# Optimization experiments

Hardware: AMD Instinct MI355X
Metric: run time of the kernel (lower is better)

## Reference

```python
import jax, jax.numpy as jnp
import numpy as np

B, S, F = 4096, 512, 128
D = 2 * F  # inner_depth = num_features * 2

def _gelu(x):
    # torch nn.GELU() default is exact (erf) form
    return jax.nn.gelu(x, approximate=False)

def setup_inputs() -> dict:
    key = jax.random.key(0)
    ks = jax.random.split(key, 10)
    w = lambda k, shp: (jax.random.normal(k, shp) * 0.05).astype(jnp.float32)
    z = lambda n: jnp.zeros((n,), jnp.float32)
    return dict(
        noise=jax.random.normal(ks[0], (B, F), dtype=jnp.float32),   # torch.randn(batch,1,F) squeezed
        eps=jax.random.normal(ks[1], (S, B, F), dtype=jnp.float32),  # rsample noise per step
        mlp_w1=w(ks[2], (F, F)), mlp_b1=z(F),
        mlp_w2=w(ks[3], (F, F)), mlp_b2=z(F),
        mlp_w3=w(ks[4], (F, F)), mlp_b3=z(F),
        hid_w=w(ks[5], (D, F)), hid_b=z(D),
        w_ih=w(ks[6], (4 * D, F)), b_ih=z(4 * D),   # PyTorch LSTM gate order: i, f, g, o
        w_hh=w(ks[7], (4 * D, D)), b_hh=z(4 * D),
        out_w=w(ks[8], (F, D)), out_b=z(F),
        z_w=w(ks[9], (2 * F, F)), z_b=z(2 * F),     # ConditionalGaussian linear -> (mu, logsigma)
        batch=B, seq_len=S,
    )

def _forward(noise, eps, mlp_w1, mlp_b1, mlp_w2, mlp_b2, mlp_w3, mlp_b3,
             hid_w, hid_b, w_ih, b_ih, w_hh, b_hh, out_w, out_b, z_w, z_b):
    # noise_mlp: Linear -> GELU -> Linear -> GELU -> Linear
    x = _gelu(noise @ mlp_w1.T + mlp_b1)
    x = _gelu(x @ mlp_w2.T + mlp_b2)
    inputs = x @ mlp_w3.T + mlp_b3          # [B, F]
    hidden = inputs @ hid_w.T + hid_b       # [B, D]
    cell = jnp.tanh(hidden)
    b = b_ih + b_hh

    def step(carry, eps_t):
        inp, h, c = carry
        gates = inp @ w_ih.T + h @ w_hh.T + b               # [B, 4D]
        i, f, g, o = jnp.split(gates, 4, axis=-1)
        c = jax.nn.sigmoid(f) * c + jax.nn.sigmoid(i) * jnp.tanh(g)
        h = jax.nn.sigmoid(o) * jnp.tanh(c)
        out = h @ out_w.T + out_b                           # [B, F]
        # ConditionalGaussian: GELU -> Linear -> chunk -> rsample (temperature=1)
        mu, logsigma = jnp.split(_gelu(out) @ z_w.T + z_b, 2, axis=-1)
        sample = mu + jnp.exp(logsigma) * eps_t             # [B, F]
        return (sample, h, c), sample

    _, ys = jax.lax.scan(step, (inputs, hidden, cell), eps)  # ys: [S, B, F]
    return jnp.transpose(ys, (1, 0, 2))  # stack(dim=1) -> [B, S, F]

def reference(noise, eps, mlp_w1, mlp_b1, mlp_w2, mlp_b2, mlp_w3, mlp_b3,
              hid_w, hid_b, w_ih, b_ih, w_hh, b_hh, out_w, out_b, z_w, z_b,
              batch, seq_len):
    return _forward(noise, eps, mlp_w1, mlp_b1, mlp_w2, mlp_b2, mlp_w3, mlp_b3,
                    hid_w, hid_b, w_ih, b_ih, w_hh, b_hh, out_w, out_b, z_w, z_b)
```

## Files before the change

kernel.cpp:

```cpp
#include <hip/hip_runtime.h>
#include <hip/hip_bf16.h>
#include <math.h>

#define BATCH 4096
#define SEQ   512
#define FDIM  128
#define DDIM  256
#define KG    384
#define NG    1024

typedef __bf16 bf16x8 __attribute__((ext_vector_type(8)));
typedef float  f32x4  __attribute__((ext_vector_type(4)));

__device__ __forceinline__ f32x4 mfma16(bf16x8 a, bf16x8 b, f32x4 c) {
    return __builtin_amdgcn_mfma_f32_16x16x32_bf16(a, b, c, 0, 0, 0);
}

__device__ __forceinline__ float rcp_(float x) { return __builtin_amdgcn_rcpf(x); }
__device__ __forceinline__ float sigmoid_(float x) { return rcp_(1.0f + __expf(-x)); }
__device__ __forceinline__ float tanh_(float x) {
    float e = __expf(-2.0f * fabsf(x));
    float t = 1.0f - 2.0f * e * rcp_(1.0f + e);
    return copysignf(t, x);
}
__device__ __forceinline__ float gelu_erf(float v) {
    return 0.5f * v * (1.0f + erff(v * 0.70710678118654752f));
}

__global__ void prep_weights(const float* __restrict__ w_ih, const float* __restrict__ w_hh,
                             const float* __restrict__ b_ih, const float* __restrict__ b_hh,
                             const float* __restrict__ out_w, const float* __restrict__ z_w,
                             __bf16* __restrict__ Wg, __bf16* __restrict__ Wout,
                             __bf16* __restrict__ Wz, float* __restrict__ bg)
{
    int i = blockIdx.x * blockDim.x + threadIdx.x;
    if (i < NG * KG) {
        int n = i / KG, k = i - n * KG;
        float v = (k < FDIM) ? w_ih[n * FDIM + k] : w_hh[n * DDIM + (k - FDIM)];
        Wg[i] = (__bf16)v;
    }
    if (i < FDIM * DDIM) Wout[i] = (__bf16)out_w[i];
    if (i < DDIM * FDIM) Wz[i]   = (__bf16)z_w[i];
    if (i < NG)          bg[i]   = b_ih[i] + b_hh[i];
}

template<int K, int N, int ACT>
__global__ void rowmlp(const float* __restrict__ x, const float* __restrict__ W,
                       const float* __restrict__ bias, float* __restrict__ y)
{
    __shared__ float xr[K];
    int m = blockIdx.x;
    for (int k = threadIdx.x; k < K; k += blockDim.x) xr[k] = x[(size_t)m * K + k];
    __syncthreads();
    for (int n = threadIdx.x; n < N; n += blockDim.x) {
        const float* wr = W + (size_t)n * K;
        float s = bias[n];
        #pragma unroll 8
        for (int k = 0; k < K; ++k) s += xr[k] * wr[k];
        if (ACT) s = gelu_erf(s);
        y[(size_t)m * N + n] = s;
    }
}

__global__ __launch_bounds__(512, 2)
void rnn_main(const float* __restrict__ eps,
              const __bf16* __restrict__ Wg, const float* __restrict__ bg,
              const __bf16* __restrict__ Wout, const float* __restrict__ ob,
              const __bf16* __restrict__ Wz, const float* __restrict__ zb,
              const float* __restrict__ x0, const float* __restrict__ h0,
              float* __restrict__ out)
{
    extern __shared__ __align__(16) char smem[];
    __bf16* xbuf  = (__bf16*)smem;
    __bf16* hbufA = xbuf  + 2048;
    __bf16* hbufB = hbufA + 4096;
    __bf16* gbuf  = hbufB + 4096;
    char*   wlds  = (char*)(gbuf + 2048);

    const int tid  = threadIdx.x;
    const int wv   = tid >> 6;
    const int lane = tid & 63;
    const int lo   = lane & 15;
    const int hi   = lane >> 4;
    const int row0 = blockIdx.x * 16;
    const int abase = (hi * 16 + lo) * 16;

    for (int e = tid; e < 16 * 128; e += 512) {
        int r = e >> 7, k = e & 127;
        xbuf[(((k >> 3) << 4) + r) * 8 + (k & 7)] = (__bf16)x0[(size_t)(row0 + r) * 128 + k];
    }
    for (int e = tid; e < 16 * 256; e += 512) {
        int r = e >> 8, k = e & 255;
        hbufA[(((k >> 3) << 4) + r) * 8 + (k & 7)] = (__bf16)h0[(size_t)(row0 + r) * 256 + k];
    }
    float c[2][4];
    #pragma unroll
    for (int p = 0; p < 2; ++p)
        #pragma unroll
        for (int j = 0; j < 4; ++j)
            c[p][j] = tanh_(h0[(size_t)(row0 + hi * 4 + j) * 256 + (2 * wv + p) * 16 + lo]);

    const __bf16* wgbase[8];
    float biasq[8];
    #pragma unroll
    for (int q = 0; q < 8; ++q) {
        int tile = (q >> 1) * 16 + 2 * wv + (q & 1);
        wgbase[q] = Wg + (size_t)(tile * 16 + lo) * KG + hi * 8;
        biasq[q]  = bg[tile * 16 + lo];
    }
    const float bo  = ob[wv * 16 + lo];
    const float bmu = zb[wv * 16 + lo];
    const float bls = zb[128 + wv * 16 + lo];

    bf16x8 wout[8];
    #pragma unroll
    for (int kt = 0; kt < 8; ++kt)
        wout[kt] = *(const bf16x8*)(Wout + (size_t)(wv * 16 + lo) * 256 + kt * 32 + hi * 8);
    bf16x8 wz0[4], wz1[4];
    #pragma unroll
    for (int kt = 0; kt < 4; ++kt) {
        wz0[kt] = *(const bf16x8*)(Wz + (size_t)(wv * 16 + lo) * 128 + kt * 32 + hi * 8);
        wz1[kt] = *(const bf16x8*)(Wz + (size_t)((8 + wv) * 16 + lo) * 128 + kt * 32 + hi * 8);
    }
    bf16x8 wgr[2][8];
    #pragma unroll
    for (int q = 0; q < 8; ++q) {
        wgr[0][q] = *(const bf16x8*)(wgbase[q] + 10 * 32);
        wgr[1][q] = *(const bf16x8*)(wgbase[q] + 11 * 32);
    }
    char* wbase = wlds + wv * 8192 + lane * 16;
    #pragma unroll
    for (int kt2 = 0; kt2 < 2; ++kt2)
        #pragma unroll
        for (int q = 0; q < 8; ++q) {
            bf16x8 w = *(const bf16x8*)(wgbase[q] + (8 + kt2) * 32);
            *(bf16x8*)(wbase + kt2 * 65536 + q * 1024) = w;
        }

    __syncthreads();

    __bf16* hb_cur = hbufA;
    __bf16* hb_nxt = hbufB;

    for (int t = 0; t < SEQ; ++t) {
        float ev[4];
        #pragma unroll
        for (int j = 0; j < 4; ++j)
            ev[j] = eps[((size_t)t * BATCH + row0 + hi * 4 + j) * 128 + wv * 16 + lo];

        f32x4 acc[8];
        #pragma unroll
        for (int q = 0; q < 8; ++q) acc[q] = (f32x4){biasq[q], biasq[q], biasq[q], biasq[q]};

        #pragma unroll 2
        for (int kt = 0; kt < 4; ++kt) {
            bf16x8 a = *(const bf16x8*)((char*)xbuf + kt * 1024 + abase);
            #pragma unroll
            for (int q = 0; q < 8; ++q) {
                bf16x8 b = *(const bf16x8*)(wgbase[q] + kt * 32);
                acc[q] = mfma16(a, b, acc[q]);
            }
        }
        #pragma unroll 2
        for (int kt = 0; kt < 4; ++kt) {
            bf16x8 a = *(const bf16x8*)((char*)hb_cur + kt * 1024 + abase);
            #pragma unroll
            for (int q = 0; q < 8; ++q) {
                bf16x8 b = *(const bf16x8*)(wgbase[q] + (4 + kt) * 32);
                acc[q] = mfma16(a, b, acc[q]);
            }
        }
        #pragma unroll
        for (int kt2 = 0; kt2 < 2; ++kt2) {
            bf16x8 a = *(const bf16x8*)((char*)hb_cur + (4 + kt2) * 1024 + abase);
            #pragma unroll
            for (int q = 0; q < 8; ++q) {
                bf16x8 b = *(const bf16x8*)(wbase + kt2 * 65536 + q * 1024);
                acc[q] = mfma16(a, b, acc[q]);
            }
        }
        #pragma unroll
        for (int kt2 = 0; kt2 < 2; ++kt2) {
            bf16x8 a = *(const bf16x8*)((char*)hb_cur + (6 + kt2) * 1024 + abase);
            #pragma unroll
            for (int q = 0; q < 8; ++q)
                acc[q] = mfma16(a, wgr[kt2][q], acc[q]);
        }

        #pragma unroll
        for (int p = 0; p < 2; ++p)
            #pragma unroll
            for (int j = 0; j < 4; ++j) {
                float iv = sigmoid_(acc[0 + p][j]);
                float fv = sigmoid_(acc[2 + p][j]);
                float gv = tanh_(acc[4 + p][j]);
                float ov = sigmoid_(acc[6 + p][j]);
                float cn = fv * c[p][j] + iv * gv;
                c[p][j] = cn;
                float hv = ov * tanh_(cn);
                int d = (2 * wv + p) * 16 + lo, r = hi * 4 + j;
                hb_nxt[(((d >> 3) << 4) + r) * 8 + (d & 7)] = (__bf16)hv;
            }
        __syncthreads();

        f32x4 ao0 = (f32x4){bo, bo, bo, bo};
        f32x4 ao1 = (f32x4){0.f, 0.f, 0.f, 0.f};
        #pragma unroll
        for (int kt = 0; kt < 4; ++kt) {
            bf16x8 a0 = *(const bf16x8*)((char*)hb_nxt + (2 * kt) * 1024 + abase);
            bf16x8 a1 = *(const bf16x8*)((char*)hb_nxt + (2 * kt + 1) * 1024 + abase);
            ao0 = mfma16(a0, wout[2 * kt], ao0);
            ao1 = mfma16(a1, wout[2 * kt + 1], ao1);
        }
        #pragma unroll
        for (int j = 0; j < 4; ++j) {
            int d = wv * 16 + lo, r = hi * 4 + j;
            gbuf[(((d >> 3) << 4) + r) * 8 + (d & 7)] = (__bf16)gelu_erf(ao0[j] + ao1[j]);
        }
        __syncthreads();

        f32x4 amu = (f32x4){bmu, bmu, bmu, bmu};
        f32x4 als = (f32x4){bls, bls, bls, bls};
        #pragma unroll
        for (int kt = 0; kt < 4; ++kt) {
            bf16x8 a = *(const bf16x8*)((char*)gbuf + kt * 1024 + abase);
            amu = mfma16(a, wz0[kt], amu);
            als = mfma16(a, wz1[kt], als);
        }
        #pragma unroll
        for (int j = 0; j < 4; ++j) {
            float smp = amu[j] + __expf(als[j]) * ev[j];
            int d = wv * 16 + lo, r = hi * 4 + j;
            xbuf[(((d >> 3) << 4) + r) * 8 + (d & 7)] = (__bf16)smp;
            out[(size_t)(row0 + r) * (SEQ * 128) + (size_t)t * 128 + d] = smp;
        }
        __syncthreads();

        __bf16* tmp = hb_cur; hb_cur = hb_nxt; hb_nxt = tmp;
    }
}

extern "C" void kernel_launch(void* const* d_in, const int* in_sizes, int n_in,
                              void* d_out, int out_size, void* d_ws, size_t ws_size,
                              hipStream_t stream)
{
    const float* noise = (const float*)d_in[0];
    const float* eps   = (const float*)d_in[1];
    const float* w1 = (const float*)d_in[2];  const float* b1 = (const float*)d_in[3];
    const float* w2 = (const float*)d_in[4];  const float* b2 = (const float*)d_in[5];
    const float* w3 = (const float*)d_in[6];  const float* b3 = (const float*)d_in[7];
    const float* hw = (const float*)d_in[8];  const float* hb = (const float*)d_in[9];
    const float* wih = (const float*)d_in[10]; const float* bih = (const float*)d_in[11];
    const float* whh = (const float*)d_in[12]; const float* bhh = (const float*)d_in[13];
    const float* ow = (const float*)d_in[14]; const float* ob = (const float*)d_in[15];
    const float* zw = (const float*)d_in[16]; const float* zb = (const float*)d_in[17];
    float* out = (float*)d_out;

    char* ws = (char*)d_ws;
    __bf16* Wg   = (__bf16*)(ws);
    __bf16* Wout = (__bf16*)(ws + 786432);
    __bf16* Wz   = (__bf16*)(ws + 851968);
    float*  bg   = (float*) (ws + 917504);
    float*  t0   = (float*) (ws + 921600);
    float*  t1   = (float*) (ws + 921600 + 2097152);
    float*  hid  = (float*) (ws + 921600 + 2 * 2097152);

    prep_weights<<<1536, 256, 0, stream>>>(wih, whh, bih, bhh, ow, zw, Wg, Wout, Wz, bg);

    rowmlp<128, 128, 1><<<4096, 128, 0, stream>>>(noise, w1, b1, t0);
    rowmlp<128, 128, 1><<<4096, 128, 0, stream>>>(t0, w2, b2, t1);
    rowmlp<128, 128, 0><<<4096, 128, 0, stream>>>(t1, w3, b3, t0);
    rowmlp<128, 256, 0><<<4096, 256, 0, stream>>>(t0, hw, hb, hid);

    rnn_main<<<256, 512, 155648, stream>>>(eps, Wg, bg, Wout, ob, Wz, zb, t0, hid, out);
}
```

Measured before the change: 9.900 ms.

## Stream gate weight k-tiles via async global-to-LDS double buffering with rotated order

Replaces direct global loads of gate weight tiles inside the MFMA loop with global_load_lds staging into two LDS buffers. Each k-tile's weights are prefetched two iterations ahead, and each block starts at a different k offset to spread L2 traffic. Barriers become lightweight lgkmcnt waits plus s_barrier, and erff is replaced by a polynomial erf approximation. This adds manual vmcnt bookkeeping, a looser GELU approximation (about 1e-7 error), and extra LDS traffic every step.

```diff
diff --git a/kernel.cpp b/kernel.cpp
--- a/kernel.cpp
+++ b/kernel.cpp
@@ -23,8 +23,16 @@
     float t = 1.0f - 2.0f * e * rcp_(1.0f + e);
     return copysignf(t, x);
 }
+__device__ __forceinline__ float erf_(float x) {
+    float ax = fabsf(x);
+    float t  = rcp_(fmaf(0.3275911f, ax, 1.0f));
+    float y  = t * fmaf(t, fmaf(t, fmaf(t, fmaf(t, 1.061405429f, -1.453152027f),
+                                        1.421413741f), -0.284496736f), 0.254829592f);
+    float r  = 1.0f - y * __expf(-ax * ax);
+    return copysignf(r, x);
+}
 __device__ __forceinline__ float gelu_erf(float v) {
-    return 0.5f * v * (1.0f + erff(v * 0.70710678118654752f));
+    return 0.5f * v * (1.0f + erf_(v * 0.70710678118654752f));
 }
 
 __global__ void prep_weights(const float* __restrict__ w_ih, const float* __restrict__ w_hh,
@@ -62,6 +70,13 @@
     }
 }
 
+__device__ __forceinline__ void bar_lds() {
+    asm volatile("s_waitcnt lgkmcnt(0)" ::: "memory");
+    __builtin_amdgcn_sched_barrier(0);
+    __builtin_amdgcn_s_barrier();
+    __builtin_amdgcn_sched_barrier(0);
+}
+
 __global__ __launch_bounds__(512, 2)
 void rnn_main(const float* __restrict__ eps,
               const __bf16* __restrict__ Wg, const float* __restrict__ bg,
@@ -72,10 +87,10 @@
 {
     extern __shared__ __align__(16) char smem[];
     __bf16* xbuf  = (__bf16*)smem;
-    __bf16* hbufA = xbuf  + 2048;
-    __bf16* hbufB = hbufA + 4096;
-    __bf16* gbuf  = hbufB + 4096;
-    char*   wlds  = (char*)(gbuf + 2048);
+    __bf16* hbufA = (__bf16*)(smem + 4096);
+    __bf16* hbufB = (__bf16*)(smem + 12288);
+    __bf16* gbuf  = (__bf16*)(smem + 20480);
+    char*   wlds  = smem + 24576;
 
     const int tid  = threadIdx.x;
     const int wv   = tid >> 6;
@@ -128,64 +143,91 @@
         wgr[0][q] = *(const bf16x8*)(wgbase[q] + 10 * 32);
         wgr[1][q] = *(const bf16x8*)(wgbase[q] + 11 * 32);
     }
-    char* wbase = wlds + wv * 8192 + lane * 16;
-    #pragma unroll
-    for (int kt2 = 0; kt2 < 2; ++kt2)
-        #pragma unroll
-        for (int q = 0; q < 8; ++q) {
-            bf16x8 w = *(const bf16x8*)(wgbase[q] + (8 + kt2) * 32);
-            *(bf16x8*)(wbase + kt2 * 65536 + q * 1024) = w;
-        }
-
+
+    const int rot = blockIdx.x % 10;
+    #define KTV(I) ((rot + (I)) < 10 ? (rot + (I)) : (rot + (I) - 10))
+    const int kt_0 = KTV(0), kt_1 = KTV(1), kt_2 = KTV(2), kt_3 = KTV(3), kt_4 = KTV(4);
+    const int kt_5 = KTV(5), kt_6 = KTV(6), kt_7 = KTV(7), kt_8 = KTV(8), kt_9 = KTV(9);
+    const int kts0 = kt_2, kts1 = kt_3, kts2 = kt_4, kts3 = kt_5, kts4 = kt_6;
+    const int kts5 = kt_7, kts6 = kt_8, kts7 = kt_9, kts8 = kt_0, kts9 = kt_1;
+
+    #define STAGE8(KTS, PAR) do {                                                         \
+        char* sd_ = wlds + (PAR) * 65536 + wv * 8192;                                     \
+        _Pragma("unroll")                                                                 \
+        for (int q = 0; q < 8; ++q) {                                                     \
+            __builtin_amdgcn_global_load_lds(                                             \
+                (const __attribute__((address_space(1))) unsigned int*)(const void*)(wgbase[q] + (KTS) * 32), \
+                (__attribute__((address_space(3))) unsigned int*)(void*)(sd_ + q * 1024), \
+                16, 0, 0);                                                                \
+        }                                                                                 \
+    } while (0)
+
+    #define GITER(I, VM) do {                                                             \
+        asm volatile("s_waitcnt vmcnt(" #VM ")" ::: "memory");                            \
+        __builtin_amdgcn_sched_barrier(0);                                                \
+        const char* rb_ = wlds + ((I) & 1) * 65536 + wv * 8192 + lane * 16;               \
+        bf16x8 a_  = *(const bf16x8*)(aptr##I + abase);                                   \
+        bf16x8 b0_ = *(const bf16x8*)(rb_ + 0 * 1024);                                    \
+        bf16x8 b1_ = *(const bf16x8*)(rb_ + 1 * 1024);                                    \
+        bf16x8 b2_ = *(const bf16x8*)(rb_ + 2 * 1024);                                    \
+        bf16x8 b3_ = *(const bf16x8*)(rb_ + 3 * 1024);                                    \
+        bf16x8 b4_ = *(const bf16x8*)(rb_ + 4 * 1024);                                    \
+        bf16x8 b5_ = *(const bf16x8*)(rb_ + 5 * 1024);                                    \
+        bf16x8 b6_ = *(const bf16x8*)(rb_ + 6 * 1024);                                    \
+        bf16x8 b7_ = *(const bf16x8*)(rb_ + 7 * 1024);                                    \
+        asm volatile("s_waitcnt lgkmcnt(0)" ::: "memory");                                \
+        __builtin_amdgcn_sched_barrier(0);                                                \
+        STAGE8(kts##I, (I) & 1);                                                          \
+        acc[0] = mfma16(a_, b0_, acc[0]);                                                 \
+        acc[1] = mfma16(a_, b1_, acc[1]);                                                 \
+        acc[2] = mfma16(a_, b2_, acc[2]);                                                 \
+        acc[3] = mfma16(a_, b3_, acc[3]);                                                 \
+        acc[4] = mfma16(a_, b4_, acc[4]);                                                 \
+        acc[5] = mfma16(a_, b5_, acc[5]);                                                 \
+        acc[6] = mfma16(a_, b6_, acc[6]);                                                 \
+        acc[7] = mfma16(a_, b7_, acc[7]);                                                 \
+    } while (0)
+
+    STAGE8(kt_0, 0);
+    STAGE8(kt_1, 1);
+    asm volatile("s_waitcnt vmcnt(0)" ::: "memory");
     __syncthreads();
 
-    __bf16* hb_cur = hbufA;
-    __bf16* hb_nxt = hbufB;
+    __bf16* hc = hbufA;
+    __bf16* hn = hbufB;
 
     for (int t = 0; t < SEQ; ++t) {
+        #define APTR(K) ((K) < 4 ? (const char*)xbuf + (K) * 1024 : (const char*)hc + ((K) - 4) * 1024)
+        const char* aptr0 = APTR(kt_0); const char* aptr1 = APTR(kt_1);
+        const char* aptr2 = APTR(kt_2); const char* aptr3 = APTR(kt_3);
+        const char* aptr4 = APTR(kt_4); const char* aptr5 = APTR(kt_5);
+        const char* aptr6 = APTR(kt_6); const char* aptr7 = APTR(kt_7);
+        const char* aptr8 = APTR(kt_8); const char* aptr9 = APTR(kt_9);
+        #undef APTR
+
         float ev[4];
         #pragma unroll
         for (int j = 0; j < 4; ++j)
             ev[j] = eps[((size_t)t * BATCH + row0 + hi * 4 + j) * 128 + wv * 16 + lo];
+        __builtin_amdgcn_sched_barrier(0);
 
         f32x4 acc[8];
         #pragma unroll
         for (int q = 0; q < 8; ++q) acc[q] = (f32x4){biasq[q], biasq[q], biasq[q], biasq[q]};
 
-        #pragma unroll 2
-        for (int kt = 0; kt < 4; ++kt) {
-            bf16x8 a = *(const bf16x8*)((char*)xbuf + kt * 1024 + abase);
+        {
+            bf16x8 a10 = *(const bf16x8*)((const char*)hc + 6 * 1024 + abase);
+            bf16x8 a11 = *(const bf16x8*)((const char*)hc + 7 * 1024 + abase);
             #pragma unroll
-            for (int q = 0; q < 8; ++q) {
-                bf16x8 b = *(const bf16x8*)(wgbase[q] + kt * 32);
-                acc[q] = mfma16(a, b, acc[q]);
-            }
-        }
-        #pragma unroll 2
-        for (int kt = 0; kt < 4; ++kt) {
-            bf16x8 a = *(const bf16x8*)((char*)hb_cur + kt * 1024 + abase);
+            for (int q = 0; q < 8; ++q) acc[q] = mfma16(a10, wgr[0][q], acc[q]);
             #pragma unroll
-            for (int q = 0; q < 8; ++q) {
-                bf16x8 b = *(const bf16x8*)(wgbase[q] + (4 + kt) * 32);
-                acc[q] = mfma16(a, b, acc[q]);
-            }
-        }
-        #pragma unroll
-        for (int kt2 = 0; kt2 < 2; ++kt2) {
-            bf16x8 a = *(const bf16x8*)((char*)hb_cur + (4 + kt2) * 1024 + abase);
-            #pragma unroll
-            for (int q = 0; q < 8; ++q) {
-                bf16x8 b = *(const bf16x8*)(wbase + kt2 * 65536 + q * 1024);
-                acc[q] = mfma16(a, b, acc[q]);
-            }
-        }
-        #pragma unroll
-        for (int kt2 = 0; kt2 < 2; ++kt2) {
-            bf16x8 a = *(const bf16x8*)((char*)hb_cur + (6 + kt2) * 1024 + abase);
-            #pragma unroll
-            for (int q = 0; q < 8; ++q)
-                acc[q] = mfma16(a, wgr[kt2][q], acc[q]);
-        }
+            for (int q = 0; q < 8; ++q) acc[q] = mfma16(a11, wgr[1][q], acc[q]);
+        }
+
+        GITER(0, 16); GITER(1, 16);
+        asm volatile("" : "+v"(ev[0]), "+v"(ev[1]), "+v"(ev[2]), "+v"(ev[3]));
+        GITER(2, 8); GITER(3, 8); GITER(4, 8); GITER(5, 8);
+        GITER(6, 8); GITER(7, 8); GITER(8, 8); GITER(9, 8);
 
         #pragma unroll
         for (int p = 0; p < 2; ++p)
@@ -199,16 +241,16 @@
                 c[p][j] = cn;
                 float hv = ov * tanh_(cn);
                 int d = (2 * wv + p) * 16 + lo, r = hi * 4 + j;
-                hb_nxt[(((d >> 3) << 4) + r) * 8 + (d & 7)] = (__bf16)hv;
+                hn[(((d >> 3) << 4) + r) * 8 + (d & 7)] = (__bf16)hv;
             }
-        __syncthreads();
+        bar_lds();
 
         f32x4 ao0 = (f32x4){bo, bo, bo, bo};
         f32x4 ao1 = (f32x4){0.f, 0.f, 0.f, 0.f};
         #pragma unroll
         for (int kt = 0; kt < 4; ++kt) {
-            bf16x8 a0 = *(const bf16x8*)((char*)hb_nxt + (2 * kt) * 1024 + abase);
-            bf16x8 a1 = *(const bf16x8*)((char*)hb_nxt + (2 * kt + 1) * 1024 + abase);
+            bf16x8 a0 = *(const bf16x8*)((const char*)hn + (2 * kt) * 1024 + abase);
+            bf16x8 a1 = *(const bf16x8*)((const char*)hn + (2 * kt + 1) * 1024 + abase);
             ao0 = mfma16(a0, wout[2 * kt], ao0);
             ao1 = mfma16(a1, wout[2 * kt + 1], ao1);
         }
@@ -217,13 +259,13 @@
             int d = wv * 16 + lo, r = hi * 4 + j;
             gbuf[(((d >> 3) << 4) + r) * 8 + (d & 7)] = (__bf16)gelu_erf(ao0[j] + ao1[j]);
         }
-        __syncthreads();
+        bar_lds();
 
         f32x4 amu = (f32x4){bmu, bmu, bmu, bmu};
         f32x4 als = (f32x4){bls, bls, bls, bls};
         #pragma unroll
         for (int kt = 0; kt < 4; ++kt) {
-            bf16x8 a = *(const bf16x8*)((char*)gbuf + kt * 1024 + abase);
+            bf16x8 a = *(const bf16x8*)((const char*)gbuf + kt * 1024 + abase);
             amu = mfma16(a, wz0[kt], amu);
             als = mfma16(a, wz1[kt], als);
         }
@@ -234,10 +276,13 @@
             xbuf[(((d >> 3) << 4) + r) * 8 + (d & 7)] = (__bf16)smp;
             out[(size_t)(row0 + r) * (SEQ * 128) + (size_t)t * 128 + d] = smp;
         }
-        __syncthreads();
-
-        __bf16* tmp = hb_cur; hb_cur = hb_nxt; hb_nxt = tmp;
-    }
+        bar_lds();
+
+        __bf16* tmp = hc; hc = hn; hn = tmp;
+    }
+    #undef GITER
+    #undef STAGE8
+    #undef KTV
 }
 
 extern "C" void kernel_launch(void* const* d_in, const int* in_sizes, int n_in,
```

Measured after the change: 18.18 ms. 1.84x slower.
